# Kernel tuning notes

Measured on AMD Instinct MI355X. Metric: run time of the kernel, lower is better.

## Reference

```python
import jax, jax.numpy as jnp
import numpy as np
from jax import lax

B, L, D_MODEL = 2, 2048, 1024
D_INNER, D_STATE, DT_RANK, D_CONV = 2048, 16, 64, 4


def setup_inputs() -> dict:
    key = jax.random.key(0)
    ks = jax.random.split(key, 10)
    s = 0.02
    A_log = jnp.log(jnp.broadcast_to(jnp.arange(1, D_STATE + 1, dtype=jnp.float32), (D_INNER, D_STATE)))
    return {
        "x": jax.random.normal(ks[0], (B, L, D_MODEL), jnp.float32),
        "in_proj_w": jax.random.normal(ks[1], (2 * D_INNER, D_MODEL), jnp.float32) * s,
        "conv_w": jax.random.normal(ks[2], (D_INNER, 1, D_CONV), jnp.float32) * s,
        "conv_b": jax.random.normal(ks[3], (D_INNER,), jnp.float32) * s,
        "x_proj_w": jax.random.normal(ks[4], (DT_RANK + 2 * D_STATE, D_INNER), jnp.float32) * s,
        "dt_proj_w": jax.random.normal(ks[5], (D_INNER, DT_RANK), jnp.float32) * s,
        "dt_proj_b": jax.random.normal(ks[6], (D_INNER,), jnp.float32) * s,
        "A_log": A_log,
        "D": jnp.ones((D_INNER,), jnp.float32),
        "out_proj_w": jax.random.normal(ks[7], (D_MODEL, D_INNER), jnp.float32) * s,
    }


def _silu(v):
    return v * jax.nn.sigmoid(v)


def _mamba_forward(x, in_proj_w, conv_w, conv_b, x_proj_w, dt_proj_w, dt_proj_b, A_log, D, out_proj_w):
    b, l, _ = x.shape
    xr = jnp.einsum('bld,ed->ble', x, in_proj_w)          # (b, l, 2*d_inner)
    xs, res = jnp.split(xr, 2, axis=-1)
    # causal depthwise conv over time
    xc = jnp.transpose(xs, (0, 2, 1))                     # (b, d_inner, l)
    xc = lax.conv_general_dilated(
        xc, conv_w, window_strides=(1,), padding=[(D_CONV - 1, 0)],
        feature_group_count=D_INNER,
        dimension_numbers=('NCH', 'OIH', 'NCH')) + conv_b[None, :, None]
    u = _silu(jnp.transpose(xc, (0, 2, 1)))               # (b, l, d_inner)
    # SSM parameters
    A = -jnp.exp(A_log)                                   # (d_inner, d_state)
    x_dbl = jnp.einsum('bld,ed->ble', u, x_proj_w)        # (b, l, dt_rank + 2*d_state)
    dt, Bm, Cm = jnp.split(x_dbl, [DT_RANK, DT_RANK + D_STATE], axis=-1)
    delta = jax.nn.softplus(jnp.einsum('blr,dr->bld', dt, dt_proj_w) + dt_proj_b)
    # discretize
    deltaA = jnp.exp(jnp.einsum('bld,dn->bldn', delta, A))        # (b, l, d_inner, d_state)
    deltaBu = jnp.einsum('bld,bln,bld->bldn', delta, Bm, u)       # (b, l, d_inner, d_state)
    # sequential selective scan over time
    def step(h, inp):
        dA, dBu, c = inp
        h = dA * h + dBu                                  # (b, d_inner, d_state)
        y = jnp.einsum('bdn,bn->bd', h, c)
        return h, y
    xs_scan = (jnp.transpose(deltaA, (1, 0, 2, 3)),
               jnp.transpose(deltaBu, (1, 0, 2, 3)),
               jnp.transpose(Cm, (1, 0, 2)))
    h0 = jnp.zeros((b, D_INNER, D_STATE), u.dtype)
    _, ys = lax.scan(step, h0, xs_scan)                   # (l, b, d_inner)
    y = jnp.transpose(ys, (1, 0, 2)) + u * D              # skip connection
    y = y * _silu(res)                                    # gate
    return jnp.einsum('bld,ed->ble', y, out_proj_w)       # (b, l, d_model)


def reference(x, in_proj_w, conv_w, conv_b, x_proj_w, dt_proj_w, dt_proj_b, A_log, D, out_proj_w):
    return _mamba_forward(x, in_proj_w, conv_w, conv_b, x_proj_w, dt_proj_w, dt_proj_b, A_log, D, out_proj_w)
```

## Files before the change

### kernel.cpp

```cpp
#include <hip/hip_runtime.h>
#include <hip/hip_bf16.h>
#include <math.h>

#define B_SZ 2
#define L_SZ 2048
#define DMODEL 1024
#define DINNER 2048
#define DSTATE 16
#define DTRANK 64
#define M_ROWS (B_SZ * L_SZ)

#define CH 32
#define CLEN (L_SZ / CH)
#define CPB 64

#define KSPLIT 8
#define KC (DINNER / KSPLIT)

typedef short shortx8 __attribute__((ext_vector_type(8)));
typedef float floatx4 __attribute__((ext_vector_type(4)));
typedef float floatx16 __attribute__((ext_vector_type(16)));

__device__ __forceinline__ float softplusf(float x) {
    return fmaxf(x, 0.f) + log1pf(expf(-fabsf(x)));
}
__device__ __forceinline__ float siluf(float x) {
    return x * (1.f / (1.f + expf(-x)));
}

__device__ __forceinline__ void async_ld16(const void* g, void* l) {
    __builtin_amdgcn_global_load_lds(
        (__attribute__((address_space(1))) void*)(unsigned long long)g,
        (__attribute__((address_space(3))) void*)(unsigned int)(unsigned long long)l,
        16, 0, 0);
}

template <int BN, int KP>
__global__ __launch_bounds__(256) void gemm_bf16_nt(
    const unsigned short* __restrict__ A,
    const unsigned short* __restrict__ Bm,
    float* __restrict__ C, int ldc)
{
    constexpr int TN32 = BN / 64;
    __shared__ unsigned short As[2 * 8192];
    __shared__ unsigned short Bs[2 * BN * 64];

    const int tid = threadIdx.x;
    const int w = tid >> 6;
    const int lane = tid & 63;
    const int wm = w >> 1, wn = w & 1;
    const int m0 = blockIdx.y * 128;
    const int n0 = blockIdx.x * BN;

    const int r4 = lane >> 2;
    const int csw = (lane & 3) ^ ((r4 >> 1) & 3);
    const int gk = csw * 8;
    const int l31 = lane & 31;
    const int khalf = lane >> 5;
    const int rsw = (l31 >> 1) & 3;

    floatx16 acc[2][TN32] = {};

    for (int k0 = 0; k0 < KP; k0 += 64) {
#pragma unroll
        for (int seg = 0; seg < 2; ++seg) {
            const unsigned short* Asrc = A + seg * KP;
            const unsigned short* Bsrc = Bm + seg * KP;
#pragma unroll
            for (int t = 0; t < 2; ++t) {
#pragma unroll
                for (int jj = 0; jj < 2; ++jj) {
                    int j = w + jj * 4;
                    async_ld16(Asrc + (size_t)(m0 + j * 16 + r4) * (2 * KP) + k0 + t * 32 + gk,
                               &As[seg * 8192 + t * 4096 + j * 512]);
                }
#pragma unroll
                for (int jj = 0; jj < BN / 64; ++jj) {
                    int j = w + jj * 4;
                    async_ld16(Bsrc + (size_t)(n0 + j * 16 + r4) * (2 * KP) + k0 + t * 32 + gk,
                               &Bs[seg * BN * 64 + t * BN * 32 + j * 512]);
                }
            }
        }
        __syncthreads();

#pragma unroll
        for (int t = 0; t < 2; ++t) {
#pragma unroll
            for (int kk = 0; kk < 2; ++kk) {
                const int pos = ((kk * 2 + khalf) ^ rsw) << 3;
                shortx8 ah[2], al[2], bh[TN32], bl[TN32];
#pragma unroll
                for (int i = 0; i < 2; ++i) {
                    int row = wm * 64 + i * 32 + l31;
                    ah[i] = *(const shortx8*)&As[t * 4096 + row * 32 + pos];
                    al[i] = *(const shortx8*)&As[8192 + t * 4096 + row * 32 + pos];
                }
#pragma unroll
                for (int j = 0; j < TN32; ++j) {
                    int col = wn * (BN / 2) + j * 32 + l31;
                    bh[j] = *(const shortx8*)&Bs[t * BN * 32 + col * 32 + pos];
                    bl[j] = *(const shortx8*)&Bs[BN * 64 + t * BN * 32 + col * 32 + pos];
                }
#pragma unroll
                for (int i = 0; i < 2; ++i)
#pragma unroll
                    for (int j = 0; j < TN32; ++j) {
                        acc[i][j] = __builtin_amdgcn_mfma_f32_32x32x16_bf16(ah[i], bh[j], acc[i][j], 0, 0, 0);
                        acc[i][j] = __builtin_amdgcn_mfma_f32_32x32x16_bf16(ah[i], bl[j], acc[i][j], 0, 0, 0);
                        acc[i][j] = __builtin_amdgcn_mfma_f32_32x32x16_bf16(al[i], bh[j], acc[i][j], 0, 0, 0);
                    }
            }
        }
        __syncthreads();
    }

#pragma unroll
    for (int i = 0; i < 2; ++i) {
#pragma unroll
        for (int j = 0; j < TN32; ++j) {
            int col = n0 + wn * (BN / 2) + j * 32 + l31;
#pragma unroll
            for (int r = 0; r < 16; ++r) {
                int row = m0 + wm * 64 + i * 32 + (r & 3) + 8 * (r >> 2) + 4 * khalf;
                C[(size_t)row * ldc + col] = acc[i][j][r];
            }
        }
    }
}

__global__ __launch_bounds__(256) void split2_kernel(
    const float* __restrict__ src, unsigned short* __restrict__ dst, int K)
{
    int i = blockIdx.x * 256 + threadIdx.x;
    int m = i / K;
    int k = i - m * K;
    float a = src[i];
    __hip_bfloat16 h = __float2bfloat16(a);
    __hip_bfloat16 l = __float2bfloat16(a - __bfloat162float(h));
    unsigned short* row = dst + (size_t)m * 2 * K;
    row[k] = *(unsigned short*)&h;
    row[K + k] = *(unsigned short*)&l;
}

__global__ __launch_bounds__(256) void xproj_splitk(
    const float* __restrict__ u, const float* __restrict__ Wx,
    float* __restrict__ Cp)
{
    __shared__ float As[16][68];
    __shared__ float Bs[16][100];

    const int tid = threadIdx.x;
    const int ks = blockIdx.x;
    const int m0 = blockIdx.y * 64;
    const int tx = tid & 15;
    const int ty = tid >> 4;

    float acc[4][6] = {};

    const int arow = tid >> 2;
    const int akk = (tid & 3) * 4;

    for (int k0 = ks * KC; k0 < (ks + 1) * KC; k0 += 16) {
        {
            float4 v = *(const float4*)&u[(size_t)(m0 + arow) * DINNER + k0 + akk];
            As[akk + 0][arow] = v.x;
            As[akk + 1][arow] = v.y;
            As[akk + 2][arow] = v.z;
            As[akk + 3][arow] = v.w;
        }
        for (int idx = tid; idx < 384; idx += 256) {
            int row = idx >> 2;
            int kk = (idx & 3) * 4;
            float4 v = *(const float4*)&Wx[(size_t)row * DINNER + k0 + kk];
            Bs[kk + 0][row] = v.x;
            Bs[kk + 1][row] = v.y;
            Bs[kk + 2][row] = v.z;
            Bs[kk + 3][row] = v.w;
        }
        __syncthreads();

#pragma unroll
        for (int k = 0; k < 16; ++k) {
            float a[4], b[6];
#pragma unroll
            for (int i = 0; i < 4; ++i) a[i] = As[k][ty * 4 + i];
#pragma unroll
            for (int j = 0; j < 6; ++j) b[j] = Bs[k][tx * 6 + j];
#pragma unroll
            for (int i = 0; i < 4; ++i)
#pragma unroll
                for (int j = 0; j < 6; ++j) acc[i][j] = fmaf(a[i], b[j], acc[i][j]);
        }
        __syncthreads();
    }

    float* outp = Cp + ((size_t)ks * M_ROWS + m0) * 96;
#pragma unroll
    for (int i = 0; i < 4; ++i)
#pragma unroll
        for (int j = 0; j < 6; ++j)
            outp[(ty * 4 + i) * 96 + tx * 6 + j] = acc[i][j];
}

__global__ __launch_bounds__(256) void xproj_reduce(
    const float* __restrict__ Cp, float* __restrict__ xdbl)
{
    int i = blockIdx.x * 256 + threadIdx.x;
    float s = 0.f;
#pragma unroll
    for (int c = 0; c < KSPLIT; ++c)
        s += Cp[(size_t)c * M_ROWS * 96 + i];
    xdbl[i] = s;
}

template <int BM, int BN, int BK, int TM, int TN, bool BOUND_N, int EPI>
__global__ __launch_bounds__(256) void gemm_nt(
    const float* __restrict__ A, int lda,
    const float* __restrict__ Bmat, int ldb,
    float* __restrict__ C, int ldc,
    int M, int N, int K, const float* __restrict__ bias)
{
    __shared__ float As[BK][BM + 4];
    __shared__ float Bs[BK][BN + 4];

    const int tid = threadIdx.x;
    const int tx = tid % (BN / TN);
    const int ty = tid / (BN / TN);
    const int m0 = blockIdx.y * BM;
    const int n0 = blockIdx.x * BN;

    float acc[TM][TN];
#pragma unroll
    for (int i = 0; i < TM; ++i)
#pragma unroll
        for (int j = 0; j < TN; ++j) acc[i][j] = 0.f;

    for (int k0 = 0; k0 < K; k0 += BK) {
        for (int idx = tid * 4; idx < BM * BK; idx += 256 * 4) {
            int row = idx / BK;
            int kk = idx % BK;
            float4 v = *(const float4*)&A[(size_t)(m0 + row) * lda + k0 + kk];
            As[kk + 0][row] = v.x;
            As[kk + 1][row] = v.y;
            As[kk + 2][row] = v.z;
            As[kk + 3][row] = v.w;
        }
        for (int idx = tid * 4; idx < BN * BK; idx += 256 * 4) {
            int row = idx / BK;
            int kk = idx % BK;
            float4 v;
            if (!BOUND_N || (n0 + row) < N)
                v = *(const float4*)&Bmat[(size_t)(n0 + row) * ldb + k0 + kk];
            else
                v = make_float4(0.f, 0.f, 0.f, 0.f);
            Bs[kk + 0][row] = v.x;
            Bs[kk + 1][row] = v.y;
            Bs[kk + 2][row] = v.z;
            Bs[kk + 3][row] = v.w;
        }
        __syncthreads();

#pragma unroll
        for (int k = 0; k < BK; ++k) {
            float a[TM], b[TN];
#pragma unroll
            for (int i = 0; i < TM; ++i) a[i] = As[k][ty * TM + i];
#pragma unroll
            for (int j = 0; j < TN; ++j) b[j] = Bs[k][tx * TN + j];
#pragma unroll
            for (int i = 0; i < TM; ++i)
#pragma unroll
                for (int j = 0; j < TN; ++j) acc[i][j] = fmaf(a[i], b[j], acc[i][j]);
        }
        __syncthreads();
    }

#pragma unroll
    for (int i = 0; i < TM; ++i) {
        int m = m0 + ty * TM + i;
#pragma unroll
        for (int j = 0; j < TN; ++j) {
            int n = n0 + tx * TN + j;
            if (BOUND_N && n >= N) continue;
            float v = acc[i][j];
            if (EPI == 1) v = softplusf(v + bias[n]);
            C[(size_t)m * ldc + n] = v;
        }
    }
}

__global__ __launch_bounds__(256) void conv_silu_v4(
    const float* __restrict__ xz, const float* __restrict__ cw,
    const float* __restrict__ cb, float* __restrict__ u)
{
    int i = blockIdx.x * 256 + threadIdx.x;
    int dq = (i & 511) << 2;
    int bl = i >> 9;
    int b = bl >> 11;
    int l = bl & 2047;

    float4 W0 = *(const float4*)&cw[(dq + 0) * 4];
    float4 W1 = *(const float4*)&cw[(dq + 1) * 4];
    float4 W2 = *(const float4*)&cw[(dq + 2) * 4];
    float4 W3 = *(const float4*)&cw[(dq + 3) * 4];
    float4 acc = *(const float4*)&cb[dq];

#pragma unroll
    for (int k = 0; k < 4; ++k) {
        int ls = l + k - 3;
        if (ls >= 0) {
            float4 v = *(const float4*)&xz[((size_t)(b << 11) + ls) * 4096 + dq];
            acc.x = fmaf(v.x, ((const float*)&W0)[k], acc.x);
            acc.y = fmaf(v.y, ((const float*)&W1)[k], acc.y);
            acc.z = fmaf(v.z, ((const float*)&W2)[k], acc.z);
            acc.w = fmaf(v.w, ((const float*)&W3)[k], acc.w);
        }
    }
    float4 r = make_float4(siluf(acc.x), siluf(acc.y), siluf(acc.z), siluf(acc.w));
    *(float4*)&u[(size_t)bl * DINNER + dq] = r;
}

template <bool PASS3>
__global__ __launch_bounds__(256) void scan_chunk(
    const float* __restrict__ dbuf, const float* __restrict__ ubuf,
    const float* __restrict__ xdbl, const float* __restrict__ A_log,
    const float* __restrict__ Dv,
    float* __restrict__ Pbuf, float* __restrict__ Sbuf,
    const float* __restrict__ xz, unsigned short* __restrict__ y2)
{
    __shared__ float sd[16][CPB];
    __shared__ float su[16][CPB];
    __shared__ float sB[16][DSTATE];
    __shared__ float sC[16][DSTATE];

    const int tid = threadIdx.x;
    const int c    = blockIdx.x % CH;
    const int dblk = (blockIdx.x / CH) % (DINNER / CPB);
    const int b    = blockIdx.x / (CH * (DINNER / CPB));
    const int d0 = dblk * CPB;
    const int dg = tid >> 2;
    const int q  = tid & 3;
    const int d  = d0 + dg;
    const size_t base_bl = (size_t)b * L_SZ + (size_t)c * CLEN;

    float Ac[4], h[4];
    float sdl = 0.f;
#pragma unroll
    for (int j = 0; j < 4; ++j)
        Ac[j] = -expf(A_log[d * DSTATE + 4 * q + j]);
    const size_t psoff = (((size_t)b * CH + c) * DINNER + d0) * DSTATE + (size_t)tid * 4;
    if (PASS3) {
        float4 h0 = *(const float4*)&Sbuf[psoff];
        h[0] = h0.x; h[1] = h0.y; h[2] = h0.z; h[3] = h0.w;
    } else {
        h[0] = h[1] = h[2] = h[3] = 0.f;
    }
    const float Dd = PASS3 ? Dv[d] : 0.f;

    const int ls = tid >> 4;
    const int g4 = (tid & 15) * 4;
    const int ln = tid & 15;

    float4 r_d = *(const float4*)&dbuf[(base_bl + ls) * DINNER + d0 + g4];
    float4 r_u = *(const float4*)&ubuf[(base_bl + ls) * DINNER + d0 + g4];
    float r_B = xdbl[(base_bl + ls) * 96 + 64 + ln];
    float r_C = xdbl[(base_bl + ls) * 96 + 80 + ln];

    for (int l0 = 0; l0 < CLEN; l0 += 16) {
        __syncthreads();
        *(float4*)&sd[ls][g4] = r_d;
        *(float4*)&su[ls][g4] = r_u;
        sB[ls][ln] = r_B;
        sC[ls][ln] = r_C;
        __syncthreads();

        if (l0 + 16 < CLEN) {
            r_d = *(const float4*)&dbuf[(base_bl + l0 + 16 + ls) * DINNER + d0 + g4];
            r_u = *(const float4*)&ubuf[(base_bl + l0 + 16 + ls) * DINNER + d0 + g4];
            r_B = xdbl[(base_bl + l0 + 16 + ls) * 96 + 64 + ln];
            r_C = xdbl[(base_bl + l0 + 16 + ls) * 96 + 80 + ln];
        }

#pragma unroll
        for (int s = 0; s < 16; ++s) {
            float dl = sd[s][dg];
            float ul = su[s][dg];
            float4 Bv = *(float4*)&sB[s][4 * q];
            float dbu = dl * ul;
            float dA0 = expf(dl * Ac[0]);
            float dA1 = expf(dl * Ac[1]);
            float dA2 = expf(dl * Ac[2]);
            float dA3 = expf(dl * Ac[3]);
            h[0] = fmaf(dA0, h[0], dbu * Bv.x);
            h[1] = fmaf(dA1, h[1], dbu * Bv.y);
            h[2] = fmaf(dA2, h[2], dbu * Bv.z);
            h[3] = fmaf(dA3, h[3], dbu * Bv.w);
            if (!PASS3) {
                sdl += dl;
            } else {
                float4 Cv = *(float4*)&sC[s][4 * q];
                float y = h[0] * Cv.x + h[1] * Cv.y + h[2] * Cv.z + h[3] * Cv.w;
                y += __shfl_xor(y, 1);
                y += __shfl_xor(y, 2);
                if (q == 0) su[s][dg] = fmaf(ul, Dd, y);
            }
        }

        if (PASS3) {
            __syncthreads();
            size_t row = base_bl + l0 + ls;
            float4 yv = *(float4*)&su[ls][g4];
            float4 rv = *(const float4*)&xz[row * 4096 + 2048 + d0 + g4];
            float a0 = yv.x * siluf(rv.x);
            float a1 = yv.y * siluf(rv.y);
            float a2 = yv.z * siluf(rv.z);
            float a3 = yv.w * siluf(rv.w);
            __hip_bfloat16 h0 = __float2bfloat16(a0), h1 = __float2bfloat16(a1);
            __hip_bfloat16 h2 = __float2bfloat16(a2), h3 = __float2bfloat16(a3);
            __hip_bfloat16 l0b = __float2bfloat16(a0 - __bfloat162float(h0));
            __hip_bfloat16 l1b = __float2bfloat16(a1 - __bfloat162float(h1));
            __hip_bfloat16 l2b = __float2bfloat16(a2 - __bfloat162float(h2));
            __hip_bfloat16 l3b = __float2bfloat16(a3 - __bfloat162float(h3));
            ushort4 hv = make_ushort4(*(unsigned short*)&h0, *(unsigned short*)&h1,
                                      *(unsigned short*)&h2, *(unsigned short*)&h3);
            ushort4 lv = make_ushort4(*(unsigned short*)&l0b, *(unsigned short*)&l1b,
                                      *(unsigned short*)&l2b, *(unsigned short*)&l3b);
            unsigned short* yrow = y2 + row * 2 * DINNER + d0 + g4;
            *(ushort4*)&yrow[0] = hv;
            *(ushort4*)&yrow[DINNER] = lv;
        }
    }

    if (!PASS3) {
        *(float4*)&Pbuf[psoff] = make_float4(expf(Ac[0] * sdl), expf(Ac[1] * sdl),
                                             expf(Ac[2] * sdl), expf(Ac[3] * sdl));
        *(float4*)&Sbuf[psoff] = make_float4(h[0], h[1], h[2], h[3]);
    }
}

__global__ __launch_bounds__(256) void scan_combine(
    const float* __restrict__ Pbuf, float* __restrict__ Sbuf)
{
    int t = blockIdx.x * 256 + threadIdx.x;
    int b = t >> 15;
    int rem = t & 32767;
    size_t base = (size_t)b * CH * DINNER * DSTATE + rem;
    float H = 0.f;
#pragma unroll 4
    for (int c = 0; c < CH; ++c) {
        size_t off = base + (size_t)c * DINNER * DSTATE;
        float S = Sbuf[off];
        float P = Pbuf[off];
        Sbuf[off] = H;
        H = fmaf(P, H, S);
    }
}

extern "C" void kernel_launch(void* const* d_in, const int* in_sizes, int n_in,
                              void* d_out, int out_size, void* d_ws, size_t ws_size,
                              hipStream_t stream)
{
    const float* x          = (const float*)d_in[0];
    const float* in_proj_w  = (const float*)d_in[1];
    const float* conv_w     = (const float*)d_in[2];
    const float* conv_b     = (const float*)d_in[3];
    const float* x_proj_w   = (const float*)d_in[4];
    const float* dt_proj_w  = (const float*)d_in[5];
    const float* dt_proj_b  = (const float*)d_in[6];
    const float* A_log      = (const float*)d_in[7];
    const float* Dv         = (const float*)d_in[8];
    const float* out_proj_w = (const float*)d_in[9];
    float* out = (float*)d_out;

    char* w = (char*)d_ws;
    float* xz   = (float*)(w);
    float* u    = (float*)(w + 67108864);
    float* dbuf = (float*)(w + 100663296);
    float* xdbl = (float*)(w + 134217728);
    float* Pbuf = (float*)(w + 135790592);
    float* Sbuf = (float*)(w + 144179200);
    unsigned short* x2  = (unsigned short*)(w + 152567808);
    unsigned short* w2a = (unsigned short*)(w + 169345024);
    unsigned short* y2  = x2;
    unsigned short* w2b = (unsigned short*)(w + 135790592);
    float* Cp = (float*)(w + 152567808);

    split2_kernel<<<(M_ROWS * DMODEL) / 256, 256, 0, stream>>>(x, x2, DMODEL);
    split2_kernel<<<(2 * DINNER * DMODEL) / 256, 256, 0, stream>>>(in_proj_w, w2a, DMODEL);
    {
        dim3 g(4096 / 128, M_ROWS / 128);
        gemm_bf16_nt<128, 1024><<<g, 256, 0, stream>>>(x2, w2a, xz, 4096);
    }
    conv_silu_v4<<<(M_ROWS * 512) / 256, 256, 0, stream>>>(xz, conv_w, conv_b, u);
    {
        dim3 g(KSPLIT, M_ROWS / 64);
        xproj_splitk<<<g, 256, 0, stream>>>(u, x_proj_w, Cp);
        xproj_reduce<<<(M_ROWS * 96) / 256, 256, 0, stream>>>(Cp, xdbl);
    }
    {
        dim3 g(2048 / 128, M_ROWS / 128);
        gemm_nt<128, 128, 16, 8, 8, false, 1><<<g, 256, 0, stream>>>(
            xdbl, 96, dt_proj_w, 64, dbuf, 2048, M_ROWS, 2048, 64, dt_proj_b);
    }
    {
        const int nblk = B_SZ * (DINNER / CPB) * CH;
        scan_chunk<false><<<nblk, 256, 0, stream>>>(dbuf, u, xdbl, A_log, Dv, Pbuf, Sbuf, nullptr, nullptr);
        scan_combine<<<B_SZ * DINNER * DSTATE / 256, 256, 0, stream>>>(Pbuf, Sbuf);
        scan_chunk<true><<<nblk, 256, 0, stream>>>(dbuf, u, xdbl, A_log, Dv, nullptr, Sbuf, xz, y2);
    }
    split2_kernel<<<(DMODEL * DINNER) / 256, 256, 0, stream>>>(out_proj_w, w2b, DINNER);
    {
        dim3 g(1024 / 64, M_ROWS / 128);
        gemm_bf16_nt<64, 2048><<<g, 256, 0, stream>>>(y2, w2b, out, 1024);
    }
}
```

Baseline: 512.2 us.

## Replace in_proj GEMM with pre-tiled 4-stage async-pipelined bf16x3 MFMA kernel

The input projection now uses a new split3 kernel that converts x and in_proj_w into bf16 hi/lo pairs laid out in a tile-contiguous packed format. It arranges the operands so the GEMM runs three bf16 passes (hi*hi, hi*lo, lo*hi) as one K=3072 stream. A new 256x256-tile GEMM with a 4-deep global_load_lds ring buffer, explicit vmcnt waits, setprio around the MFMA block and a swizzled workgroup order consumes this packed data. The aim is to hide global latency and improve data reuse with larger tiles. The cost is a single workgroup per CU (64K shorts of LDS) and only 256 workgroups.

New measurement: 548.5 us. 7.1% more time.

```diff
diff --git a/kernel.cpp b/kernel.cpp
--- a/kernel.cpp
+++ b/kernel.cpp
@@ -33,6 +33,137 @@
         (__attribute__((address_space(1))) void*)(unsigned long long)g,
         (__attribute__((address_space(3))) void*)(unsigned int)(unsigned long long)l,
         16, 0, 0);
+}
+
+
+template <int LO>
+__global__ __launch_bounds__(256) void split3_kernel(
+    const float* __restrict__ src, unsigned short* __restrict__ dst)
+{
+    int i = blockIdx.x * 256 + threadIdx.x;
+    int row = i & 4095;
+    int k8 = i >> 12;
+    const float* s = src + (size_t)row * 1024 + k8 * 8;
+    float4 v0 = *(const float4*)s;
+    float4 v1 = *(const float4*)(s + 4);
+    float vs[8] = {v0.x, v0.y, v0.z, v0.w, v1.x, v1.y, v1.z, v1.w};
+    unsigned short hs[8], ls[8];
+#pragma unroll
+    for (int j = 0; j < 8; ++j) {
+        __hip_bfloat16 h = __float2bfloat16(vs[j]);
+        __hip_bfloat16 l = __float2bfloat16(vs[j] - __bfloat162float(h));
+        hs[j] = *(unsigned short*)&h;
+        ls[j] = *(unsigned short*)&l;
+    }
+    shortx8 hv = *(shortx8*)hs;
+    shortx8 lv = *(shortx8*)ls;
+    int p = row >> 8, rr = row & 255;
+    size_t b0 = ((size_t)(p * 96 + (k8 >> 2)) * 4 + (k8 & 3)) * 2048 + rr * 8;
+    *(shortx8*)&dst[b0]          = hv;
+    *(shortx8*)&dst[b0 + 262144] = (LO == 1) ? lv : hv;
+    *(shortx8*)&dst[b0 + 524288] = (LO == 1) ? hv : lv;
+}
+
+template <int KT, int NB>
+__global__ __launch_bounds__(256, 1) void gemm_pipe_bf16(
+    const unsigned short* __restrict__ Ap,
+    const unsigned short* __restrict__ Bp,
+    float* __restrict__ C, int ldc)
+{
+    __shared__ unsigned short lds[65536];
+
+    const int tid = threadIdx.x;
+    const int w = tid >> 6;
+    const int lane = tid & 63;
+    const int wm = w >> 1, wn = w & 1;
+    const int l31 = lane & 31, lh = lane >> 5;
+
+    int nwg = gridDim.x;
+    int id = blockIdx.x;
+    id = (id & 7) * (nwg >> 3) + (id >> 3);
+    const int bm = id / NB;
+    const int bn = id % NB;
+
+    const unsigned short* ga = Ap + (size_t)bm * KT * 8192;
+    const unsigned short* gb = Bp + (size_t)bn * KT * 8192;
+    const int soff = w * 512 + lane * 8;
+
+#pragma unroll
+    for (int t = 0; t < 3; ++t) {
+        unsigned short* lb = lds + t * 16384;
+        const size_t go = (size_t)t * 8192;
+#pragma unroll
+        for (int c = 0; c < 4; ++c) {
+            async_ld16(ga + go + c * 2048 + soff, lb + c * 2048 + w * 512);
+            async_ld16(gb + go + c * 2048 + soff, lb + 8192 + c * 2048 + w * 512);
+        }
+    }
+    asm volatile("s_waitcnt vmcnt(16)" ::: "memory");
+    __builtin_amdgcn_s_barrier();
+
+    const int arow = (wm * 128 + l31) * 8;
+    const int brow = (wn * 128 + l31) * 8;
+    floatx16 acc[4][4] = {};
+
+    for (int t = 0; t < KT; ++t) {
+        if (t + 3 < KT) {
+            unsigned short* sb = lds + ((t + 3) & 3) * 16384;
+            const size_t go = (size_t)(t + 3) * 8192;
+#pragma unroll
+            for (int c = 0; c < 4; ++c) {
+                async_ld16(ga + go + c * 2048 + soff, sb + c * 2048 + w * 512);
+                async_ld16(gb + go + c * 2048 + soff, sb + 8192 + c * 2048 + w * 512);
+            }
+        }
+        const unsigned short* lb = lds + (t & 3) * 16384;
+        __builtin_amdgcn_s_setprio(1);
+#pragma unroll
+        for (int ks = 0; ks < 2; ++ks) {
+            const int slab = (ks * 2 + lh) * 2048;
+            shortx8 a0 = *(const shortx8*)&lb[slab + arow];
+            shortx8 a1 = *(const shortx8*)&lb[slab + arow + 256];
+            shortx8 a2 = *(const shortx8*)&lb[slab + arow + 512];
+            shortx8 a3 = *(const shortx8*)&lb[slab + arow + 768];
+            shortx8 b0 = *(const shortx8*)&lb[8192 + slab + brow];
+            shortx8 b1 = *(const shortx8*)&lb[8192 + slab + brow + 256];
+            shortx8 b2 = *(const shortx8*)&lb[8192 + slab + brow + 512];
+            shortx8 b3 = *(const shortx8*)&lb[8192 + slab + brow + 768];
+            acc[0][0] = __builtin_amdgcn_mfma_f32_32x32x16_bf16(a0, b0, acc[0][0], 0, 0, 0);
+            acc[0][1] = __builtin_amdgcn_mfma_f32_32x32x16_bf16(a0, b1, acc[0][1], 0, 0, 0);
+            acc[0][2] = __builtin_amdgcn_mfma_f32_32x32x16_bf16(a0, b2, acc[0][2], 0, 0, 0);
+            acc[0][3] = __builtin_amdgcn_mfma_f32_32x32x16_bf16(a0, b3, acc[0][3], 0, 0, 0);
+            acc[1][0] = __builtin_amdgcn_mfma_f32_32x32x16_bf16(a1, b0, acc[1][0], 0, 0, 0);
+            acc[1][1] = __builtin_amdgcn_mfma_f32_32x32x16_bf16(a1, b1, acc[1][1], 0, 0, 0);
+            acc[1][2] = __builtin_amdgcn_mfma_f32_32x32x16_bf16(a1, b2, acc[1][2], 0, 0, 0);
+            acc[1][3] = __builtin_amdgcn_mfma_f32_32x32x16_bf16(a1, b3, acc[1][3], 0, 0, 0);
+            acc[2][0] = __builtin_amdgcn_mfma_f32_32x32x16_bf16(a2, b0, acc[2][0], 0, 0, 0);
+            acc[2][1] = __builtin_amdgcn_mfma_f32_32x32x16_bf16(a2, b1, acc[2][1], 0, 0, 0);
+            acc[2][2] = __builtin_amdgcn_mfma_f32_32x32x16_bf16(a2, b2, acc[2][2], 0, 0, 0);
+            acc[2][3] = __builtin_amdgcn_mfma_f32_32x32x16_bf16(a2, b3, acc[2][3], 0, 0, 0);
+            acc[3][0] = __builtin_amdgcn_mfma_f32_32x32x16_bf16(a3, b0, acc[3][0], 0, 0, 0);
+            acc[3][1] = __builtin_amdgcn_mfma_f32_32x32x16_bf16(a3, b1, acc[3][1], 0, 0, 0);
+            acc[3][2] = __builtin_amdgcn_mfma_f32_32x32x16_bf16(a3, b2, acc[3][2], 0, 0, 0);
+            acc[3][3] = __builtin_amdgcn_mfma_f32_32x32x16_bf16(a3, b3, acc[3][3], 0, 0, 0);
+        }
+        __builtin_amdgcn_s_setprio(0);
+        if (t < KT - 3)       { asm volatile("s_waitcnt vmcnt(16)" ::: "memory"); }
+        else if (t == KT - 3) { asm volatile("s_waitcnt vmcnt(8)"  ::: "memory"); }
+        else if (t == KT - 2) { asm volatile("s_waitcnt vmcnt(0)"  ::: "memory"); }
+        __builtin_amdgcn_s_barrier();
+    }
+
+#pragma unroll
+    for (int i = 0; i < 4; ++i) {
+#pragma unroll
+        for (int j = 0; j < 4; ++j) {
+            int col = bn * 256 + wn * 128 + j * 32 + l31;
+#pragma unroll
+            for (int r = 0; r < 16; ++r) {
+                int row = bm * 256 + wm * 128 + i * 32 + (r & 3) + 8 * (r >> 2) + 4 * lh;
+                C[(size_t)row * ldc + col] = acc[i][j][r];
+            }
+        }
+    }
 }
 
 template <int BN, int KP>
@@ -480,18 +611,15 @@
     float* xdbl = (float*)(w + 134217728);
     float* Pbuf = (float*)(w + 135790592);
     float* Sbuf = (float*)(w + 144179200);
-    unsigned short* x2  = (unsigned short*)(w + 152567808);
-    unsigned short* w2a = (unsigned short*)(w + 169345024);
-    unsigned short* y2  = x2;
+    unsigned short* y2  = (unsigned short*)(w + 152567808);
     unsigned short* w2b = (unsigned short*)(w + 135790592);
     float* Cp = (float*)(w + 152567808);
-
-    split2_kernel<<<(M_ROWS * DMODEL) / 256, 256, 0, stream>>>(x, x2, DMODEL);
-    split2_kernel<<<(2 * DINNER * DMODEL) / 256, 256, 0, stream>>>(in_proj_w, w2a, DMODEL);
-    {
-        dim3 g(4096 / 128, M_ROWS / 128);
-        gemm_bf16_nt<128, 1024><<<g, 256, 0, stream>>>(x2, w2a, xz, 4096);
-    }
+    unsigned short* x2p  = (unsigned short*)(w + 67108864);
+    unsigned short* w2ap = (unsigned short*)(w + 100663296);
+
+    split3_kernel<1><<<2048, 256, 0, stream>>>(x, x2p);
+    split3_kernel<2><<<2048, 256, 0, stream>>>(in_proj_w, w2ap);
+    gemm_pipe_bf16<96, 16><<<256, 256, 0, stream>>>(x2p, w2ap, xz, 4096);
     conv_silu_v4<<<(M_ROWS * 512) / 256, 256, 0, stream>>>(xz, conv_w, conv_b, u);
     {
         dim3 g(KSPLIT, M_ROWS / 64);
```

## Replace in_proj GEMM with 256x256 8-phase pipelined bf16x3 MFMA kernel

Applied to the files above, without the earlier changes.

The in_proj GEMM gets a new 512-thread kernel with 256x256 tiles. It runs an 8-phase software pipeline that issues async global-to-LDS loads between MFMA groups, uses barrier and priority hints, and swizzles block ids. A new split kernel writes the hi/lo bf16 pieces of the inputs straight into a pre-tiled layout, so the three bf16 products (hi*hi, lo*hi, hi*lo) can be streamed as 48 K-tiles. This aims to raise MFMA utilisation and cut LDS staging overhead, at the cost of a large register footprint and a hard-coded shape-specific layout.

New measurement: 613.9 us. +19.8%, slower.

```diff
diff --git a/kernel.cpp b/kernel.cpp
--- a/kernel.cpp
+++ b/kernel.cpp
@@ -33,6 +33,155 @@
         (__attribute__((address_space(1))) void*)(unsigned long long)g,
         (__attribute__((address_space(3))) void*)(unsigned int)(unsigned long long)l,
         16, 0, 0);
+}
+
+
+template <int LO>
+__global__ __launch_bounds__(256) void split3_kernel(
+    const float* __restrict__ src, unsigned short* __restrict__ dst)
+{
+    int i = blockIdx.x * 256 + threadIdx.x;
+    int row = i & 4095;
+    int k8s = i >> 12;
+    const float* s = src + (size_t)row * 1024 + k8s * 8;
+    float4 v0 = *(const float4*)s;
+    float4 v1 = *(const float4*)(s + 4);
+    float vs[8] = {v0.x, v0.y, v0.z, v0.w, v1.x, v1.y, v1.z, v1.w};
+    unsigned short hsv[8], lsv[8];
+#pragma unroll
+    for (int j = 0; j < 8; ++j) {
+        __hip_bfloat16 h = __float2bfloat16(vs[j]);
+        __hip_bfloat16 l = __float2bfloat16(vs[j] - __bfloat162float(h));
+        hsv[j] = *(unsigned short*)&h;
+        lsv[j] = *(unsigned short*)&l;
+    }
+    shortx8 hv = *(shortx8*)hsv;
+    shortx8 lv = *(shortx8*)lsv;
+    int p = row >> 8, rr = row & 255;
+    int tloc = k8s >> 3;
+    int sh = (k8s >> 2) & 1;
+    int k8l = k8s & 3;
+    size_t unit = (size_t)(k8l * 256 + rr) * 8;
+#pragma unroll
+    for (int e = 0; e < 3; ++e) {
+        int T = e * 16 + tloc;
+        size_t off = (size_t)(p * 96 + T * 2 + sh) * 8192 + unit;
+        shortx8 val = (LO == 1) ? (e == 1 ? lv : hv) : (e == 2 ? lv : hv);
+        *(shortx8*)&dst[off] = val;
+    }
+}
+
+template <int KT>
+__global__ __launch_bounds__(512, 2) void gemm_8ph(
+    const unsigned short* __restrict__ Ap,
+    const unsigned short* __restrict__ Bp,
+    float* __restrict__ C, int ldc)
+{
+    __shared__ unsigned short lds[65536];
+
+    const int tid = threadIdx.x;
+    const int lane = tid & 63;
+    const int w = tid >> 6;
+    const int wm = w >> 2, wn = w & 3;
+    const int l15 = lane & 15, l4 = lane >> 4;
+
+    int id = blockIdx.x;
+    id = (id & 7) * 32 + (id >> 3);
+    const int bm = id >> 4, bn = id & 15;
+
+    const unsigned short* ga = Ap + (size_t)bm * KT * 16384;
+    const unsigned short* gb = Bp + (size_t)bn * KT * 16384;
+
+    const int rA = (l4 * 256 + wm * 128 + l15) * 8;
+    const int rB = (l4 * 256 + wn * 64 + l15) * 8;
+
+    floatx4 acc[8][4] = {};
+    shortx8 bfr[4];
+
+    auto STAGE = [&](int vt, int ab, int s) {
+        int T = vt < KT ? vt : KT - 1;
+        const unsigned short* src = (ab ? gb : ga) + ((size_t)T * 2 + s) * 8192 + tid * 8;
+        unsigned short* dst = (unsigned short*)lds + (vt & 1) * 32768 + ab * 16384 + s * 8192 + tid * 8;
+        async_ld16(src, dst);
+        async_ld16(src + 4096, dst + 4096);
+    };
+
+#define MFMA16(MH)                                                                             \
+    acc[(MH)*4+0][0] = __builtin_amdgcn_mfma_f32_16x16x32_bf16(af0, bfr[0], acc[(MH)*4+0][0], 0,0,0); \
+    acc[(MH)*4+0][1] = __builtin_amdgcn_mfma_f32_16x16x32_bf16(af0, bfr[1], acc[(MH)*4+0][1], 0,0,0); \
+    acc[(MH)*4+0][2] = __builtin_amdgcn_mfma_f32_16x16x32_bf16(af0, bfr[2], acc[(MH)*4+0][2], 0,0,0); \
+    acc[(MH)*4+0][3] = __builtin_amdgcn_mfma_f32_16x16x32_bf16(af0, bfr[3], acc[(MH)*4+0][3], 0,0,0); \
+    acc[(MH)*4+1][0] = __builtin_amdgcn_mfma_f32_16x16x32_bf16(af1, bfr[0], acc[(MH)*4+1][0], 0,0,0); \
+    acc[(MH)*4+1][1] = __builtin_amdgcn_mfma_f32_16x16x32_bf16(af1, bfr[1], acc[(MH)*4+1][1], 0,0,0); \
+    acc[(MH)*4+1][2] = __builtin_amdgcn_mfma_f32_16x16x32_bf16(af1, bfr[2], acc[(MH)*4+1][2], 0,0,0); \
+    acc[(MH)*4+1][3] = __builtin_amdgcn_mfma_f32_16x16x32_bf16(af1, bfr[3], acc[(MH)*4+1][3], 0,0,0); \
+    acc[(MH)*4+2][0] = __builtin_amdgcn_mfma_f32_16x16x32_bf16(af2, bfr[0], acc[(MH)*4+2][0], 0,0,0); \
+    acc[(MH)*4+2][1] = __builtin_amdgcn_mfma_f32_16x16x32_bf16(af2, bfr[1], acc[(MH)*4+2][1], 0,0,0); \
+    acc[(MH)*4+2][2] = __builtin_amdgcn_mfma_f32_16x16x32_bf16(af2, bfr[2], acc[(MH)*4+2][2], 0,0,0); \
+    acc[(MH)*4+2][3] = __builtin_amdgcn_mfma_f32_16x16x32_bf16(af2, bfr[3], acc[(MH)*4+2][3], 0,0,0); \
+    acc[(MH)*4+3][0] = __builtin_amdgcn_mfma_f32_16x16x32_bf16(af3, bfr[0], acc[(MH)*4+3][0], 0,0,0); \
+    acc[(MH)*4+3][1] = __builtin_amdgcn_mfma_f32_16x16x32_bf16(af3, bfr[1], acc[(MH)*4+3][1], 0,0,0); \
+    acc[(MH)*4+3][2] = __builtin_amdgcn_mfma_f32_16x16x32_bf16(af3, bfr[2], acc[(MH)*4+3][2], 0,0,0); \
+    acc[(MH)*4+3][3] = __builtin_amdgcn_mfma_f32_16x16x32_bf16(af3, bfr[3], acc[(MH)*4+3][3], 0,0,0);
+
+#define PHASE(SLOT, S, MH, SVT, SAB, SS, DO_VM)                                \
+    {                                                                          \
+        const unsigned short* Ab = &lds[(SLOT)*32768 + (S)*8192] + rA;         \
+        shortx8 af0 = *(const shortx8*)&Ab[((MH)*4 + 0) * 128];                \
+        shortx8 af1 = *(const shortx8*)&Ab[((MH)*4 + 1) * 128];                \
+        shortx8 af2 = *(const shortx8*)&Ab[((MH)*4 + 2) * 128];                \
+        shortx8 af3 = *(const shortx8*)&Ab[((MH)*4 + 3) * 128];                \
+        if ((MH) == 0) {                                                       \
+            const unsigned short* Bb = &lds[(SLOT)*32768 + 16384 + (S)*8192] + rB; \
+            bfr[0] = *(const shortx8*)&Bb[0];                                  \
+            bfr[1] = *(const shortx8*)&Bb[128];                                \
+            bfr[2] = *(const shortx8*)&Bb[256];                                \
+            bfr[3] = *(const shortx8*)&Bb[384];                                \
+        }                                                                      \
+        STAGE(SVT, SAB, SS);                                                   \
+        __builtin_amdgcn_s_barrier();                                          \
+        asm volatile("s_waitcnt lgkmcnt(0)" ::: "memory");                     \
+        __builtin_amdgcn_s_setprio(1);                                         \
+        MFMA16(MH)                                                             \
+        __builtin_amdgcn_s_setprio(0);                                         \
+        if (DO_VM) { asm volatile("s_waitcnt vmcnt(8)" ::: "memory"); }        \
+        __builtin_amdgcn_s_barrier();                                          \
+    }
+
+    STAGE(0, 0, 0); STAGE(0, 1, 0); STAGE(0, 0, 1); STAGE(0, 1, 1);
+    STAGE(1, 0, 0); STAGE(1, 1, 0);
+    asm volatile("s_waitcnt vmcnt(8)" ::: "memory");
+    __builtin_amdgcn_s_barrier();
+
+#pragma unroll 1
+    for (int i = 0; i < KT / 2; ++i) {
+        const int t2 = 2 * i;
+        PHASE(0, 0, 0, t2 + 1, 0, 1, 0)
+        PHASE(0, 0, 1, t2 + 1, 1, 1, 1)
+        PHASE(0, 1, 0, t2 + 2, 0, 0, 0)
+        PHASE(0, 1, 1, t2 + 2, 1, 0, 1)
+        PHASE(1, 0, 0, t2 + 2, 0, 1, 0)
+        PHASE(1, 0, 1, t2 + 2, 1, 1, 1)
+        PHASE(1, 1, 0, t2 + 3, 0, 0, 0)
+        PHASE(1, 1, 1, t2 + 3, 1, 0, 1)
+    }
+
+#undef PHASE
+#undef MFMA16
+
+    const int c0 = bn * 256 + wn * 64;
+    const int r0 = bm * 256 + wm * 128;
+#pragma unroll
+    for (int fi = 0; fi < 8; ++fi) {
+#pragma unroll
+        for (int fj = 0; fj < 4; ++fj) {
+            int col = c0 + fj * 16 + l15;
+            int rowb = r0 + fi * 16 + l4 * 4;
+#pragma unroll
+            for (int ri = 0; ri < 4; ++ri)
+                C[(size_t)(rowb + ri) * ldc + col] = acc[fi][fj][ri];
+        }
+    }
 }
 
 template <int BN, int KP>
@@ -480,18 +629,15 @@
     float* xdbl = (float*)(w + 134217728);
     float* Pbuf = (float*)(w + 135790592);
     float* Sbuf = (float*)(w + 144179200);
-    unsigned short* x2  = (unsigned short*)(w + 152567808);
-    unsigned short* w2a = (unsigned short*)(w + 169345024);
-    unsigned short* y2  = x2;
+    unsigned short* y2  = (unsigned short*)(w + 152567808);
     unsigned short* w2b = (unsigned short*)(w + 135790592);
     float* Cp = (float*)(w + 152567808);
-
-    split2_kernel<<<(M_ROWS * DMODEL) / 256, 256, 0, stream>>>(x, x2, DMODEL);
-    split2_kernel<<<(2 * DINNER * DMODEL) / 256, 256, 0, stream>>>(in_proj_w, w2a, DMODEL);
-    {
-        dim3 g(4096 / 128, M_ROWS / 128);
-        gemm_bf16_nt<128, 1024><<<g, 256, 0, stream>>>(x2, w2a, xz, 4096);
-    }
+    unsigned short* x2p  = (unsigned short*)(w + 67108864);
+    unsigned short* w2ap = (unsigned short*)(w + 100663296);
+
+    split3_kernel<1><<<2048, 256, 0, stream>>>(x, x2p);
+    split3_kernel<2><<<2048, 256, 0, stream>>>(in_proj_w, w2ap);
+    gemm_8ph<48><<<256, 512, 0, stream>>>(x2p, w2ap, xz, 4096);
     conv_silu_v4<<<(M_ROWS * 512) / 256, 256, 0, stream>>>(xz, conv_w, conv_b, u);
     {
         dim3 g(KSPLIT, M_ROWS / 64);
```
